# Kernel optimization log

Hardware: AMD Instinct MI355X
Metric: run time of the kernel (lower is better)

Reference implementation:

```python
import jax, jax.numpy as jnp
import numpy as np
from jax import lax

ALPHA = 2.0  # ATan surrogate alpha (spikingjelly default)
V_TH = 1.0   # threshold; v_reset = 0.0 (hard reset)

@jax.custom_vjp
def spike_fn(x):
    return (x >= 0.0).astype(x.dtype)

def _spike_fwd(x):
    return spike_fn(x), x

def _spike_bwd(x, g):
    # ATan surrogate: alpha/2 / (1 + (pi/2*alpha*x)^2)
    sg = (ALPHA / 2.0) / (1.0 + (jnp.pi / 2.0 * ALPHA * x) ** 2)
    return (g * sg,)

spike_fn.defvjp(_spike_fwd, _spike_bwd)

def conv_bn(x_seq, w, gamma, beta, mean, var, eps=1e-5):
    # x_seq: [T,B,C,H,W]; conv+BN applied over flattened T*B (SeqToANNContainer)
    T, B, C, H, W = x_seq.shape
    y = lax.conv_general_dilated(
        x_seq.reshape(T * B, C, H, W), w,
        window_strides=(1, 1), padding='SAME',
        dimension_numbers=('NCHW', 'OIHW', 'NCHW'))
    inv = gamma / jnp.sqrt(var + eps)
    y = y * inv[None, :, None, None] + (beta - mean * inv)[None, :, None, None]
    Co = w.shape[0]
    return y.reshape(T, B, Co, H, W)

def plif(x_seq, w):
    # Parametric LIF: v <- v + (x - v) * sigmoid(w); hard reset to 0; detach_reset
    k = jax.nn.sigmoid(w)
    def step(v, x):
        v = v + (x - v) * k
        s = spike_fn(v - V_TH)
        v = v * (1.0 - lax.stop_gradient(s))
        return v, s
    _, s_seq = lax.scan(step, jnp.zeros_like(x_seq[0]), x_seq)
    return s_seq

def setup_inputs() -> dict:
    key = jax.random.key(0)
    ks = jax.random.split(key, 4)
    T, B, C, H, W = 4, 8, 128, 56, 56
    mid = 128
    x = (jax.random.uniform(ks[0], (T, B, C, H, W), jnp.float32) < 0.5).astype(jnp.float32)
    conv1_w = jax.random.normal(ks[1], (mid, C, 3, 3), jnp.float32) * (1.0 / np.sqrt(C * 9))
    conv2_w = jax.random.normal(ks[2], (C, mid, 3, 3), jnp.float32) * (1.0 / np.sqrt(mid * 9))
    return {
        'x': x,
        'conv1_w': conv1_w,
        'gamma1': jnp.ones((mid,), jnp.float32), 'beta1': jnp.zeros((mid,), jnp.float32),
        'mean1': jnp.zeros((mid,), jnp.float32), 'var1': jnp.ones((mid,), jnp.float32),
        'w1': jnp.float32(0.0),  # init_tau=2.0 -> w = -log(tau-1) = 0
        'conv2_w': conv2_w,
        'gamma2': jnp.ones((C,), jnp.float32), 'beta2': jnp.zeros((C,), jnp.float32),
        'mean2': jnp.zeros((C,), jnp.float32), 'var2': jnp.ones((C,), jnp.float32),
        'w2': jnp.float32(0.0),
    }

def reference(x, conv1_w, gamma1, beta1, mean1, var1, w1,
              conv2_w, gamma2, beta2, mean2, var2, w2):
    s1 = plif(conv_bn(x, conv1_w, gamma1, beta1, mean1, var1), w1)
    s2 = plif(conv_bn(s1, conv2_w, gamma2, beta2, mean2, var2), w2)
    out = s2 + x  # connect_f == 'ADD'
    return out
```

## Files before the change

kernel.cpp:

```cpp
#include <hip/hip_runtime.h>
#include <math.h>

#define T_ 4
#define B_ 8
#define C_ 128
#define H_ 56
#define W_ 56
#define NIMG (T_ * B_)
#define HW (H_ * W_)
#define NLOC ((size_t)B_ * C_ * HW)
#define NE ((size_t)T_ * NLOC)
#define APITCH 8448

typedef __attribute__((ext_vector_type(4))) int   int4v;

#define GLOAD_LDS16(gp, lp) \
    __builtin_amdgcn_global_load_lds((const __attribute__((address_space(1))) unsigned int*)(gp), \
                                     (__attribute__((address_space(3))) unsigned int*)(lp), 16, 0, 0)

__global__ __launch_bounds__(128) void scale_k(const float* __restrict__ w,
                                               float* __restrict__ sv) {
    __shared__ float red[128];
    int co = blockIdx.x, t = threadIdx.x;
    const float* p = w + (size_t)co * 1152 + t * 9;
    float m = 0.f;
#pragma unroll
    for (int j = 0; j < 9; ++j) m = fmaxf(m, fabsf(p[j]));
    red[t] = m; __syncthreads();
    for (int off = 64; off; off >>= 1) {
        if (t < off) red[t] = fmaxf(red[t], red[t + off]);
        __syncthreads();
    }
    if (t == 0) sv[co] = fmaxf(red[0], 1e-20f) / 127.f;
}

__global__ __launch_bounds__(256) void repack_k(const float* __restrict__ w,
                                                const float* __restrict__ sv,
                                                signed char* __restrict__ Bs) {
    int idx = blockIdx.x * 256 + threadIdx.x;
    if (idx >= 9 * 1024) return;
    int tap = idx >> 10;
    int rem = idx & 1023;
    int co = rem >> 3, cig = rem & 7;
    double s = (double)sv[co];
    union { signed char b[16]; int4v v; } q[3];
#pragma unroll
    for (int e = 0; e < 16; ++e) {
        int ci = cig * 16 + e;
        double v = (double)w[((size_t)co * 128 + ci) * 9 + tap];
        double q1 = rint(v / s);
        double r1 = v - s * q1;
        double q2 = rint(r1 * 128.0 / s);
        double r2 = r1 - s * q2 * 0.0078125;
        double q3 = rint(r2 * 16384.0 / s);
        q[0].b[e] = (signed char)(int)q1;
        q[1].b[e] = (signed char)(int)q2;
        q[2].b[e] = (signed char)(int)q3;
    }
    int Lb = co * 128 + ((cig ^ (co & 7)) << 4);
#pragma unroll
    for (int sp = 0; sp < 3; ++sp)
        *(int4v*)(Bs + (size_t)(tap * 3 + sp) * 16384 + Lb) = q[sp].v;
}

__global__ __launch_bounds__(256) void xpose_k(const float* __restrict__ x,
                                               signed char* __restrict__ Xt) {
    __shared__ float xs[128][57];
    int n = blockIdx.x / 56, h = blockIdx.x % 56;
    int tid = threadIdx.x;
    const float* xp = x + (size_t)n * 128 * HW + h * 56;
#pragma unroll
    for (int j = 0; j < 7; ++j) {
        int idx = tid + j * 256;
        int c = idx / 14, wq = idx - c * 14;
        float4 v = *(const float4*)(xp + (size_t)c * HW + wq * 4);
        xs[c][wq * 4 + 0] = v.x; xs[c][wq * 4 + 1] = v.y;
        xs[c][wq * 4 + 2] = v.z; xs[c][wq * 4 + 3] = v.w;
    }
    __syncthreads();
    signed char* Op = Xt + ((size_t)n * HW + h * 56) * 128;
#pragma unroll
    for (int j = 0; j < 2; ++j) {
        int idx = tid + j * 256;
        if (idx < 448) {
            int ww = idx >> 3, sl = idx & 7;
            int cg = sl ^ (ww & 7);
            union { signed char b[16]; int4v v; } u;
#pragma unroll
            for (int e = 0; e < 16; ++e)
                u.b[e] = (xs[cg * 16 + e][ww] >= 0.5f) ? 1 : 0;
            *(int4v*)(Op + ww * 128 + sl * 16) = u.v;
        }
    }
}

template<int MODE>
__global__ __launch_bounds__(512) void convplif_k(
        const signed char* __restrict__ Xin,
        const signed char* __restrict__ Bs,
        const float* __restrict__ sv,
        const float* __restrict__ gamma, const float* __restrict__ beta,
        const float* __restrict__ mean,  const float* __restrict__ var,
        const float* __restrict__ tau,
        const float* __restrict__ xres,
        void* __restrict__ outp) {
    __shared__ signed char aA[4 * APITCH];
    __shared__ signed char bB[2][49152];
    __shared__ signed char sS[2 * 8192];

    const int tid = threadIdx.x;
    const int lane = tid & 63;
    const int wave = tid >> 6;
    const int fr = lane & 15, fq = lane >> 4;
    const int row_local = wave >> 2;
    const int q = wave & 3;
    const int bb = blockIdx.x / 28;
    const int h0 = (blockIdx.x % 28) * 2;
    const int h = h0 + row_local;
    const int tap0 = (int)((blockIdx.x * 4u) % 9u);
    const int nA = (h0 == 0 || h0 == 54) ? 3 : 4;

    const float kk = 1.f / (1.f + expf(-tau[0]));
    float mulv[2], bsv[2];
#pragma unroll
    for (int nf = 0; nf < 2; ++nf) {
        int co = q * 32 + nf * 16 + fr;
        float iv = gamma[co] / sqrtf(var[co] + 1e-5f);
        mulv[nf] = sv[co] * iv;
        bsv[nf] = beta[co] - mean[co] * iv;
    }

    const int4v zi = (int4v){0, 0, 0, 0};

#define STAGEA(tt) do {                                                           \
        const signed char* _XtN = Xin + (size_t)((tt) * 8 + bb) * (HW * 128);     \
        if (tid < 448) {                                                          \
            _Pragma("unroll")                                                     \
            for (int _i = 0; _i < 4; ++_i) {                                      \
                int _hh = h0 - 1 + _i;                                            \
                if ((unsigned)_hh < 56u)                                          \
                    GLOAD_LDS16((const char*)(_XtN + (size_t)_hh * 7168) + tid * 16, \
                                (char*)aA + _i * APITCH + 128 + tid * 16);        \
            }                                                                     \
        }                                                                         \
    } while (0)

#define STAGEB(tp, buf) do {                                                      \
        const char* _src = (const char*)Bs + (size_t)(tp) * 49152 + tid * 16;     \
        char* _dst = (char*)&bB[(buf)][0] + tid * 16;                             \
        _Pragma("unroll")                                                         \
        for (int _c = 0; _c < 6; ++_c)                                            \
            GLOAD_LDS16(_src + _c * 8192, _dst + _c * 8192);                      \
    } while (0)

#define LOADA(tp) do {                                                            \
        const int _dh = (tp) / 3, _dw = (tp) - ((tp) / 3) * 3;                    \
        const signed char* _rb = aA + (row_local + _dh) * APITCH;                 \
        _Pragma("unroll")                                                         \
        for (int _m = 0; _m < 4; ++_m) {                                          \
            int _px1 = _m * 16 + fr + _dw;                                        \
            int _k7 = (_px1 - 1) & 7;                                             \
            const signed char* _bp = _rb + _px1 * 128;                            \
            a[_m][0] = *(const int4v*)(_bp + ((fq ^ _k7) << 4));                  \
            a[_m][1] = *(const int4v*)(_bp + (((4 + fq) ^ _k7) << 4));            \
        }                                                                         \
    } while (0)

    for (int j = tid; j < 320; j += 512) {
        int row = j / 80, off = j - (j / 80) * 80;
        int byte = row * APITCH + (off < 8 ? off * 16 : 7296 + (off - 8) * 16);
        *(int4v*)((char*)aA + byte) = zi;
    }
    if (h0 == 0)
        for (int j = tid; j < 528; j += 512) *(int4v*)((char*)aA + j * 16) = zi;
    if (h0 == 54)
        for (int j = tid; j < 528; j += 512) *(int4v*)((char*)aA + 3 * APITCH + j * 16) = zi;
    STAGEA(0);
    STAGEB(tap0, 0);
    asm volatile("s_waitcnt vmcnt(0) lgkmcnt(0)" ::: "memory");
    __builtin_amdgcn_sched_barrier(0);
    __builtin_amdgcn_s_barrier();

    int4v acc[3][4][2];
#pragma unroll
    for (int sp = 0; sp < 3; ++sp)
#pragma unroll
        for (int m = 0; m < 4; ++m) { acc[sp][m][0] = zi; acc[sp][m][1] = zi; }
    float v[2][4][4];
#pragma unroll
    for (int nf = 0; nf < 2; ++nf)
#pragma unroll
        for (int m = 0; m < 4; ++m)
#pragma unroll
            for (int r = 0; r < 4; ++r) v[nf][m][r] = 0.f;
    int4v a[4][2];
    LOADA(tap0);

    const int cob = (q * 32 + fr) * 128;
    const int sl0 = (fq ^ (fr & 7)) << 4;
    const int sl1 = ((4 + fq) ^ (fr & 7)) << 4;

    int tap = tap0;
    for (int g = 0; g < 36; ++g) {
        const int t = g / 9;
        const int it = g - t * 9;
        const bool tend = (it == 8);
        const int ntap = (tap + 1 == 9) ? 0 : tap + 1;

        if (tend && t < 3) STAGEA(t + 1);
        if (g < 35) STAGEB(ntap, (g + 1) & 1);
        if (g == 35) {
            asm volatile("s_waitcnt vmcnt(0)" ::: "memory");
        } else if (tend) {
            if (tid < 448) {
                if (nA == 4) asm volatile("s_waitcnt vmcnt(10)" ::: "memory");
                else         asm volatile("s_waitcnt vmcnt(9)"  ::: "memory");
            } else {
                asm volatile("s_waitcnt vmcnt(6)" ::: "memory");
            }
        } else {
            asm volatile("s_waitcnt vmcnt(6)" ::: "memory");
        }
        __builtin_amdgcn_sched_barrier(0);
        __builtin_amdgcn_s_barrier();

        const signed char* bbase = &bB[g & 1][0];
        int4v bfr[3][2][2];
#pragma unroll
        for (int sp = 0; sp < 3; ++sp) {
            const signed char* bp = bbase + sp * 16384;
            bfr[sp][0][0] = *(const int4v*)(bp + cob + sl0);
            bfr[sp][1][0] = *(const int4v*)(bp + cob + sl1);
            bfr[sp][0][1] = *(const int4v*)(bp + cob + 2048 + sl0);
            bfr[sp][1][1] = *(const int4v*)(bp + cob + 2048 + sl1);
        }
        if (it == 0 && g > 0) LOADA(tap);

        const bool dotail = !tend;
        const int ndh = ntap / 3, ndw = ntap - ndh * 3;
        const signed char* nrb = aA + (row_local + ndh) * APITCH;

        __builtin_amdgcn_s_setprio(1);
#pragma unroll
        for (int m = 0; m < 4; ++m) {
#pragma unroll
            for (int sp = 0; sp < 3; ++sp) {
                acc[sp][m][0] = __builtin_amdgcn_mfma_i32_16x16x64_i8(a[m][0], bfr[sp][0][0], acc[sp][m][0], 0, 0, 0);
                acc[sp][m][1] = __builtin_amdgcn_mfma_i32_16x16x64_i8(a[m][0], bfr[sp][0][1], acc[sp][m][1], 0, 0, 0);
            }
#pragma unroll
            for (int sp = 0; sp < 3; ++sp) {
                acc[sp][m][0] = __builtin_amdgcn_mfma_i32_16x16x64_i8(a[m][1], bfr[sp][1][0], acc[sp][m][0], 0, 0, 0);
                acc[sp][m][1] = __builtin_amdgcn_mfma_i32_16x16x64_i8(a[m][1], bfr[sp][1][1], acc[sp][m][1], 0, 0, 0);
            }
            if (dotail) {
                int px1 = m * 16 + fr + ndw;
                int k7 = (px1 - 1) & 7;
                const signed char* bp2 = nrb + px1 * 128;
                a[m][0] = *(const int4v*)(bp2 + ((fq ^ k7) << 4));
                a[m][1] = *(const int4v*)(bp2 + (((4 + fq) ^ k7) << 4));
            }
        }
        __builtin_amdgcn_s_setprio(0);

        if (it == 7) {
            asm volatile("s_waitcnt lgkmcnt(0)" ::: "memory");
            __builtin_amdgcn_sched_barrier(0);
        }
        __builtin_amdgcn_s_barrier();

        if (tend) {
            if (MODE == 0) {
                signed char* S1 = (signed char*)outp;
#pragma unroll
                for (int nf = 0; nf < 2; ++nf)
#pragma unroll
                    for (int m = 0; m < 4; ++m)
#pragma unroll
                        for (int r = 0; r < 4; ++r) {
                            int px = m * 16 + fq * 4 + r;
                            float val = (float)acc[0][m][nf][r]
                                      + (float)acc[1][m][nf][r] * 0.0078125f
                                      + (float)acc[2][m][nf][r] * 6.103515625e-05f;
                            float y = fmaf(val, mulv[nf], bsv[nf]);
                            float vv = v[nf][m][r];
                            vv = vv + (y - vv) * kk;
                            bool spk = vv >= 1.f;
                            v[nf][m][r] = spk ? 0.f : vv;
                            sS[row_local * 8192 + px * 128 + q * 32 + nf * 16 + fr] = spk ? 1 : 0;
                        }
                asm volatile("s_waitcnt lgkmcnt(0)" ::: "memory");
                __builtin_amdgcn_s_barrier();
                const size_t imgb = (size_t)(t * 8 + bb) * HW;
#pragma unroll
                for (int cc = 0; cc < 2; ++cc) {
                    int chunk = tid + cc * 512;
                    int row = chunk >> 9, rem = chunk & 511;
                    int px = rem >> 3, cg = rem & 7;
                    if (px < 56) {
                        int4v v16 = *(const int4v*)(sS + row * 8192 + px * 128 + cg * 16);
                        *(int4v*)(S1 + (imgb + (size_t)(h0 + row) * 56 + px) * 128
                                     + ((cg ^ (px & 7)) << 4)) = v16;
                    }
                }
            } else {
                float* outw = (float*)outp;
#pragma unroll
                for (int nf = 0; nf < 2; ++nf) {
                    const size_t cobase = ((size_t)(t * 8 + bb) * 128 + q * 32 + nf * 16 + fr) * HW
                                        + (size_t)h * 56;
#pragma unroll
                    for (int m = 0; m < 4; ++m) {
                        int px0 = m * 16 + fq * 4;
                        float o4[4];
#pragma unroll
                        for (int r = 0; r < 4; ++r) {
                            float val = (float)acc[0][m][nf][r]
                                      + (float)acc[1][m][nf][r] * 0.0078125f
                                      + (float)acc[2][m][nf][r] * 6.103515625e-05f;
                            float y = fmaf(val, mulv[nf], bsv[nf]);
                            float vv = v[nf][m][r];
                            vv = vv + (y - vv) * kk;
                            bool spk = vv >= 1.f;
                            v[nf][m][r] = spk ? 0.f : vv;
                            o4[r] = spk ? 1.f : 0.f;
                        }
                        if (px0 < 56) {
                            float4 xv = *(const float4*)(xres + cobase + px0);
                            float4 ov = make_float4(o4[0] + xv.x, o4[1] + xv.y,
                                                    o4[2] + xv.z, o4[3] + xv.w);
                            *(float4*)(outw + cobase + px0) = ov;
                        }
                    }
                }
            }
#pragma unroll
            for (int sp = 0; sp < 3; ++sp)
#pragma unroll
                for (int m = 0; m < 4; ++m) { acc[sp][m][0] = zi; acc[sp][m][1] = zi; }
        }
        tap = ntap;
    }
#undef STAGEA
#undef STAGEB
#undef LOADA
}

extern "C" void kernel_launch(void* const* d_in, const int* in_sizes, int n_in,
                              void* d_out, int out_size, void* d_ws, size_t ws_size,
                              hipStream_t stream) {
    const float* x    = (const float*)d_in[0];
    const float* w1   = (const float*)d_in[1];
    const float* g1   = (const float*)d_in[2];
    const float* be1  = (const float*)d_in[3];
    const float* mu1  = (const float*)d_in[4];
    const float* va1  = (const float*)d_in[5];
    const float* tau1 = (const float*)d_in[6];
    const float* w2   = (const float*)d_in[7];
    const float* g2   = (const float*)d_in[8];
    const float* be2  = (const float*)d_in[9];
    const float* mu2  = (const float*)d_in[10];
    const float* va2  = (const float*)d_in[11];
    const float* tau2 = (const float*)d_in[12];
    float* out = (float*)d_out;

    char* ws = (char*)d_ws;
    signed char* Xt  = (signed char*)ws;
    signed char* S1  = (signed char*)(ws + NE);
    float* sv1  = (float*)(ws + 2 * NE);
    float* sv2  = sv1 + 128;
    signed char* Bs1 = (signed char*)(ws + 2 * NE + 1024);
    signed char* Bs2 = Bs1 + 27 * 16384;

    scale_k<<<128, 128, 0, stream>>>(w1, sv1);
    scale_k<<<128, 128, 0, stream>>>(w2, sv2);
    repack_k<<<36, 256, 0, stream>>>(w1, sv1, Bs1);
    repack_k<<<36, 256, 0, stream>>>(w2, sv2, Bs2);
    xpose_k<<<NIMG * 56, 256, 0, stream>>>(x, Xt);

    convplif_k<0><<<B_ * 28, 512, 0, stream>>>(Xt, Bs1, sv1, g1, be1, mu1, va1,
                                               tau1, x, (void*)S1);
    convplif_k<1><<<B_ * 28, 512, 0, stream>>>(S1, Bs2, sv2, g2, be2, mu2, va2,
                                               tau2, x, (void*)out);
}
```

Measured before the change: 161.0 us.

## Prefetch B fragments into registers one tap ahead and deepen B staging

Global-to-LDS staging of weight tiles now runs two taps ahead instead of one, and the B operand fragments are read from LDS into registers for the next tap while the current tap's MFMAs execute, interleaved per spatial split. This is meant to hide LDS read latency for the B fragments that previously stalled at the start of every tap. It adds a full lgkmcnt wait and an extra barrier each iteration, holds more B registers, and reorders the MFMA loop, which could lower occupancy or add synchronization overhead.

```diff
diff --git a/kernel.cpp b/kernel.cpp
--- a/kernel.cpp
+++ b/kernel.cpp
@@ -177,6 +177,7 @@
         for (int j = tid; j < 528; j += 512) *(int4v*)((char*)aA + 3 * APITCH + j * 16) = zi;
     STAGEA(0);
     STAGEB(tap0, 0);
+    STAGEB((tap0 + 1) % 9, 1);
     asm volatile("s_waitcnt vmcnt(0) lgkmcnt(0)" ::: "memory");
     __builtin_amdgcn_sched_barrier(0);
     __builtin_amdgcn_s_barrier();
@@ -193,25 +194,42 @@
         for (int m = 0; m < 4; ++m)
 #pragma unroll
             for (int r = 0; r < 4; ++r) v[nf][m][r] = 0.f;
-    int4v a[4][2];
-    LOADA(tap0);
 
     const int cob = (q * 32 + fr) * 128;
     const int sl0 = (fq ^ (fr & 7)) << 4;
     const int sl1 = ((4 + fq) ^ (fr & 7)) << 4;
 
-    int tap = tap0;
+    int4v a[4][2];
+    int4v b[3][4];
+    LOADA(tap0);
+    {
+        const signed char* bbase = &bB[0][0];
+#pragma unroll
+        for (int sp = 0; sp < 3; ++sp) {
+            const signed char* bp = bbase + sp * 16384;
+            b[sp][0] = *(const int4v*)(bp + cob + sl0);
+            b[sp][1] = *(const int4v*)(bp + cob + sl1);
+            b[sp][2] = *(const int4v*)(bp + cob + 2048 + sl0);
+            b[sp][3] = *(const int4v*)(bp + cob + 2048 + sl1);
+        }
+    }
+    asm volatile("s_waitcnt lgkmcnt(0)" ::: "memory");
+    __builtin_amdgcn_sched_barrier(0);
+    __builtin_amdgcn_s_barrier();
+
     for (int g = 0; g < 36; ++g) {
         const int t = g / 9;
         const int it = g - t * 9;
         const bool tend = (it == 8);
+        const int tap = (tap0 + g) % 9;
         const int ntap = (tap + 1 == 9) ? 0 : tap + 1;
 
         if (tend && t < 3) STAGEA(t + 1);
-        if (g < 35) STAGEB(ntap, (g + 1) & 1);
-        if (g == 35) {
+        if (g <= 33) STAGEB((tap0 + g + 2) % 9, g & 1);
+
+        if (g >= 34) {
             asm volatile("s_waitcnt vmcnt(0)" ::: "memory");
-        } else if (tend) {
+        } else if (tend && t < 3) {
             if (tid < 448) {
                 if (nA == 4) asm volatile("s_waitcnt vmcnt(10)" ::: "memory");
                 else         asm volatile("s_waitcnt vmcnt(9)"  ::: "memory");
@@ -224,49 +242,43 @@
         __builtin_amdgcn_sched_barrier(0);
         __builtin_amdgcn_s_barrier();
 
-        const signed char* bbase = &bB[g & 1][0];
-        int4v bfr[3][2][2];
-#pragma unroll
-        for (int sp = 0; sp < 3; ++sp) {
-            const signed char* bp = bbase + sp * 16384;
-            bfr[sp][0][0] = *(const int4v*)(bp + cob + sl0);
-            bfr[sp][1][0] = *(const int4v*)(bp + cob + sl1);
-            bfr[sp][0][1] = *(const int4v*)(bp + cob + 2048 + sl0);
-            bfr[sp][1][1] = *(const int4v*)(bp + cob + 2048 + sl1);
-        }
         if (it == 0 && g > 0) LOADA(tap);
 
-        const bool dotail = !tend;
+        const bool datail = (it != 8) && (g < 35);
+        const bool dbtail = (g < 35);
         const int ndh = ntap / 3, ndw = ntap - ndh * 3;
         const signed char* nrb = aA + (row_local + ndh) * APITCH;
+        const signed char* nb = &bB[(g + 1) & 1][0];
 
         __builtin_amdgcn_s_setprio(1);
 #pragma unroll
-        for (int m = 0; m < 4; ++m) {
-#pragma unroll
-            for (int sp = 0; sp < 3; ++sp) {
-                acc[sp][m][0] = __builtin_amdgcn_mfma_i32_16x16x64_i8(a[m][0], bfr[sp][0][0], acc[sp][m][0], 0, 0, 0);
-                acc[sp][m][1] = __builtin_amdgcn_mfma_i32_16x16x64_i8(a[m][0], bfr[sp][0][1], acc[sp][m][1], 0, 0, 0);
+        for (int sp = 0; sp < 3; ++sp) {
+#pragma unroll
+            for (int m = 0; m < 4; ++m) {
+                acc[sp][m][0] = __builtin_amdgcn_mfma_i32_16x16x64_i8(a[m][0], b[sp][0], acc[sp][m][0], 0, 0, 0);
+                acc[sp][m][0] = __builtin_amdgcn_mfma_i32_16x16x64_i8(a[m][1], b[sp][1], acc[sp][m][0], 0, 0, 0);
+                acc[sp][m][1] = __builtin_amdgcn_mfma_i32_16x16x64_i8(a[m][0], b[sp][2], acc[sp][m][1], 0, 0, 0);
+                acc[sp][m][1] = __builtin_amdgcn_mfma_i32_16x16x64_i8(a[m][1], b[sp][3], acc[sp][m][1], 0, 0, 0);
+                if (sp == 2 && datail) {
+                    int px1 = m * 16 + fr + ndw;
+                    int k7 = (px1 - 1) & 7;
+                    const signed char* bp2 = nrb + px1 * 128;
+                    a[m][0] = *(const int4v*)(bp2 + ((fq ^ k7) << 4));
+                    a[m][1] = *(const int4v*)(bp2 + (((4 + fq) ^ k7) << 4));
+                }
             }
-#pragma unroll
-            for (int sp = 0; sp < 3; ++sp) {
-                acc[sp][m][0] = __builtin_amdgcn_mfma_i32_16x16x64_i8(a[m][1], bfr[sp][1][0], acc[sp][m][0], 0, 0, 0);
-                acc[sp][m][1] = __builtin_amdgcn_mfma_i32_16x16x64_i8(a[m][1], bfr[sp][1][1], acc[sp][m][1], 0, 0, 0);
+            if (dbtail) {
+                const signed char* bp2 = nb + sp * 16384;
+                b[sp][0] = *(const int4v*)(bp2 + cob + sl0);
+                b[sp][1] = *(const int4v*)(bp2 + cob + sl1);
+                b[sp][2] = *(const int4v*)(bp2 + cob + 2048 + sl0);
+                b[sp][3] = *(const int4v*)(bp2 + cob + 2048 + sl1);
             }
-            if (dotail) {
-                int px1 = m * 16 + fr + ndw;
-                int k7 = (px1 - 1) & 7;
-                const signed char* bp2 = nrb + px1 * 128;
-                a[m][0] = *(const int4v*)(bp2 + ((fq ^ k7) << 4));
-                a[m][1] = *(const int4v*)(bp2 + (((4 + fq) ^ k7) << 4));
-            }
         }
         __builtin_amdgcn_s_setprio(0);
 
-        if (it == 7) {
-            asm volatile("s_waitcnt lgkmcnt(0)" ::: "memory");
-            __builtin_amdgcn_sched_barrier(0);
-        }
+        asm volatile("s_waitcnt lgkmcnt(0)" ::: "memory");
+        __builtin_amdgcn_sched_barrier(0);
         __builtin_amdgcn_s_barrier();
 
         if (tend) {
@@ -303,6 +315,7 @@
                                      + ((cg ^ (px & 7)) << 4)) = v16;
                     }
                 }
+                __builtin_amdgcn_s_barrier();
             } else {
                 float* outw = (float*)outp;
 #pragma unroll
@@ -339,7 +352,6 @@
 #pragma unroll
                 for (int m = 0; m < 4; ++m) { acc[sp][m][0] = zi; acc[sp][m][1] = zi; }
         }
-        tap = ntap;
     }
 #undef STAGEA
 #undef STAGEB
```

Result: no change. 163.4 us, median of 3 (+1.5%).
